# Optimization experiments

Hardware: AMD Instinct MI355X
Metric: run time of the kernel (lower is better)

The kernel has to match this reference:

```python
import jax, jax.numpy as jnp
import numpy as np

T, B, V, L = 2000, 64, 163, 200  # frames, batch, vocab (162 phonemes + blank), max label len
NEG = -1e30  # log-space 'zero'
BLANK = 0


def _logaddexp3(a, b, c):
    m = jnp.maximum(jnp.maximum(a, b), c)
    return m + jnp.log(jnp.exp(a - m) + jnp.exp(b - m) + jnp.exp(c - m))


def _ctc_single(logp, labels, act_len, label_len):
    # logp: [T, V] log-probs for one utterance; labels: [L] ints in [1, V)
    Tt, _ = logp.shape
    Ll = labels.shape[0]
    S = 2 * Ll + 1  # extended label: blank, l1, blank, l2, ..., blank
    s = jnp.arange(S)
    ext = jnp.where(s % 2 == 1, labels[jnp.minimum((s - 1) // 2, Ll - 1)], BLANK)
    valid = s < 2 * label_len + 1
    ext_m2 = jnp.concatenate([jnp.full((2,), -1, ext.dtype), ext[:-2]])
    allow_skip = (ext != BLANK) & (ext != ext_m2)

    alpha0 = jnp.where((s < 2) & valid, logp[0, ext], NEG)

    def step(alpha, tlp):
        t, lp = tlp
        sh1 = jnp.concatenate([jnp.full((1,), NEG, alpha.dtype), alpha[:-1]])
        sh2 = jnp.concatenate([jnp.full((2,), NEG, alpha.dtype), alpha[:-2]])
        sh2 = jnp.where(allow_skip, sh2, NEG)
        new = _logaddexp3(alpha, sh1, sh2) + lp[ext]
        new = jnp.where(valid, new, NEG)
        new = jnp.where(t < act_len, new, alpha)  # freeze past this utterance's length
        return new, None

    ts = jnp.arange(1, Tt)
    alpha, _ = jax.lax.scan(step, alpha0, (ts, logp[1:]))

    end = 2 * label_len  # index of final blank
    a_last = alpha[end]
    a_prev = jnp.where(label_len > 0, alpha[jnp.maximum(end - 1, 0)], NEG)
    m = jnp.maximum(a_last, a_prev)
    ll = m + jnp.log(jnp.exp(a_last - m) + jnp.exp(a_prev - m))
    return -ll  # negative log-likelihood


def setup_inputs() -> dict:
    key = jax.random.key(0)
    k1, k2, k3, k4 = jax.random.split(key, 4)
    logits = jax.random.normal(k1, (T, B, V), dtype=jnp.float32)
    # labels in [1, V): module does IntTensor(concat(phonemes)) + 1, blank = 0
    labels = jax.random.randint(k2, (B, L), 0, V - 1, dtype=jnp.int32) + 1
    label_lens = jax.random.randint(k3, (B,), L // 2, L + 1, dtype=jnp.int32)
    act_lens = jax.random.randint(k4, (B,), T // 2, T + 1, dtype=jnp.int32)
    # module enforces act_len > label_len (always true here: >=1000 vs <=200)
    return {"logits": logits, "labels": labels, "act_lens": act_lens, "label_lens": label_lens}


def reference(logits, labels, act_lens, label_lens):
    # warp-ctc applies softmax internally over the vocab axis
    logp = jax.nn.log_softmax(logits, axis=-1)          # [T, B, V]
    logp_b = jnp.transpose(logp, (1, 0, 2))             # [B, T, V]
    losses = jax.vmap(_ctc_single)(logp_b, labels, act_lens, label_lens)  # [B]
    # warp-ctc length_average=True: sum of losses / total number of frames
    total = jnp.sum(losses) / jnp.sum(act_lens).astype(losses.dtype)
    return total
```

## Files before the change

kernel.cpp:

```cpp
#include <hip/hip_runtime.h>
#include <math.h>

#define T_FRAMES 2000
#define B_BATCH  64
#define V_VOCAB  163
#define L_MAX    200
#define SPT      8
#define EBIAS    320
#define PFD      8
#define GROW     260

#define L2E 1.4426950408889634f
#define LN2D 0.6931471805599453

typedef float f4 __attribute__((ext_vector_type(4)));

__device__ __forceinline__ float wave_reduce_max(float v) {
#pragma unroll
  for (int i = 1; i < 64; i <<= 1) v = fmaxf(v, __shfl_xor(v, i, 64));
  return v;
}
__device__ __forceinline__ float wave_reduce_sum(float v) {
#pragma unroll
  for (int i = 1; i < 64; i <<= 1) v += __shfl_xor(v, i, 64);
  return v;
}
__device__ __forceinline__ int wave_reduce_max_i(int v) {
#pragma unroll
  for (int i = 1; i < 64; i <<= 1) v = max(v, __shfl_xor(v, i, 64));
  return v;
}
__device__ __forceinline__ double wave_reduce_sum_d(double v) {
#pragma unroll
  for (int i = 1; i < 64; i <<= 1) v += __shfl_xor(v, i, 64);
  return v;
}

__global__ __launch_bounds__(256) void softmax_expand_kernel(const float* __restrict__ logits,
                                                             const int* __restrict__ labels,
                                                             float* __restrict__ G) {
  int r = blockIdx.x * 4 + (threadIdx.x >> 6);
  int lane = threadIdx.x & 63;
  int w = threadIdx.x >> 6;
  int b = r / T_FRAMES;
  int t = r - b * T_FRAMES;
  const float* __restrict__ src = logits + ((size_t)t * B_BATCH + b) * V_VOCAB;
  float x0 = (lane < V_VOCAB) ? src[lane] : -1e30f;
  float x1 = (lane + 64 < V_VOCAB) ? src[lane + 64] : -1e30f;
  float x2 = (lane + 128 < V_VOCAB) ? src[lane + 128] : -1e30f;
  float e0 = exp2f(fmaf(x0, L2E, -12.0f));
  float e1 = exp2f(fmaf(x1, L2E, -12.0f));
  float e2 = exp2f(fmaf(x2, L2E, -12.0f));
  float inv = 1.0f / wave_reduce_sum(e0 + e1 + e2);

  __shared__ float pl[4][V_VOCAB];
  if (lane < V_VOCAB) pl[w][lane] = e0 * inv;
  if (lane + 64 < V_VOCAB) pl[w][lane + 64] = e1 * inv;
  if (lane + 128 < V_VOCAB) pl[w][lane + 128] = e2 * inv;
  __syncthreads();

  const int* __restrict__ lb = labels + b * L_MAX;
  float* __restrict__ dst = G + (size_t)r * GROW;
  int k0 = lane * 4;
  f4 o;
#pragma unroll
  for (int i = 0; i < 4; ++i) {
    int k = k0 + i;
    int kc = (k < L_MAX) ? k : (L_MAX - 1);
    o[i] = pl[w][lb[kc]];
  }
  *(f4*)(dst + k0) = o;
  if (lane == 0) dst[256] = pl[w][0];
}

__global__ __launch_bounds__(256) void lse_kernel(const float* __restrict__ logits,
                                                  float* __restrict__ lse2) {
  int row = blockIdx.x * 4 + (threadIdx.x >> 6);
  if (row >= T_FRAMES * B_BATCH) return;
  int lane = threadIdx.x & 63;
  const float* __restrict__ src = logits + (size_t)row * V_VOCAB;
  float x0 = (lane < V_VOCAB) ? src[lane] : -1e30f;
  float x1 = (lane + 64 < V_VOCAB) ? src[lane + 64] : -1e30f;
  float x2 = (lane + 128 < V_VOCAB) ? src[lane + 128] : -1e30f;
  float mx = wave_reduce_max(fmaxf(fmaxf(x0, x1), x2));
  float ssum = wave_reduce_sum(exp2f((x0 - mx) * L2E) + exp2f((x1 - mx) * L2E) +
                               exp2f((x2 - mx) * L2E));
  if (lane == 0) lse2[row] = mx * L2E + log2f(ssum);
}

__device__ __forceinline__ void gload4(f4& dst, int voff, const float* sbase) {
  asm volatile("global_load_dwordx4 %0, %1, %2"
               : "=v"(dst)
               : "v"(voff), "s"(sbase));
}
__device__ __forceinline__ void gload1(float& dst, int voff, const float* sbase) {
  asm volatile("global_load_dword %0, %1, %2"
               : "=v"(dst)
               : "v"(voff), "s"(sbase));
}
template <int N>
__device__ __forceinline__ void wait_row2(f4& q, float& bl) {
  asm volatile("s_waitcnt vmcnt(%2)" : "+v"(q), "+v"(bl) : "i"(N));
}
template <int N>
__device__ __forceinline__ void wait_row3(f4& q, float& bl, float& p4) {
  asm volatile("s_waitcnt vmcnt(%3)" : "+v"(q), "+v"(bl), "+v"(p4) : "i"(N));
}

__global__ __launch_bounds__(64, 1) void ctc_bidir_kernel(const float* __restrict__ G,
                                                          const int* __restrict__ labels,
                                                          const int* __restrict__ act_lens,
                                                          const int* __restrict__ label_lens,
                                                          double* __restrict__ Am,
                                                          double* __restrict__ Bm,
                                                          int* __restrict__ LSa,
                                                          int* __restrict__ LSb) {
  const int bid = blockIdx.x;
  const bool fwd = bid < B_BATCH;
  const int b = fwd ? bid : bid - B_BATCH;
  const int lane = threadIdx.x;
  const int act_len = act_lens[b];
  const int LL = label_lens[b];
  const int send = 2 * LL;
  const int tm = act_len >> 1;
  const int* __restrict__ lb = labels + b * L_MAX;
  const float* __restrict__ base = G + (size_t)b * T_FRAMES * GROW;

  const int voff4 = lane * 16;
  const int voffb = 256 * 4;
  const int voffp = lane * 16 + 16;

  f4 Q[PFD];
  float BL[PFD];
  double a[SPT];
  int LS = 0;

  if (fwd) {
    double m2o[4];
#pragma unroll
    for (int jj = 0; jj < 4; ++jj) {
      int k = 4 * lane + jj;
      int kc = (k < L_MAX) ? k : (L_MAX - 1);
      int kp = (k - 1 < L_MAX) ? (k - 1) : (L_MAX - 1);
      m2o[jj] = (k >= 1 && lb[kc] != lb[kp]) ? 1.0 : 0.0;
    }
    const double m10 = (lane == 0) ? 0.0 : 1.0;

#pragma unroll
    for (int j = 0; j < SPT; ++j) a[j] = 0.0;
    if (lane == 0) {
      a[0] = (double)base[256];
      a[1] = (double)base[0];
    }
    asm volatile("s_waitcnt vmcnt(0)" ::: "memory");

    const float* bp = base + GROW;
    const float* bhi = base + (size_t)(T_FRAMES - 1) * GROW;
    auto issue = [&](int p) {
      const float* rp = (bp > bhi) ? bhi : bp;
      gload4(Q[p], voff4, rp);
      gload1(BL[p], voffb, rp);
      bp += GROW;
    };

    double prev1;
    auto step = [&](int p) {
      double B = (double)BL[p];
      double p1 = (double)Q[p][0], p3 = (double)Q[p][1];
      double p5 = (double)Q[p][2], p7 = (double)Q[p][3];
      double n6 = (a[6] + a[5]) * B;
      double n7 = fma(m2o[3], a[5], a[7] + a[6]) * p7;
      double np1 = __shfl_up(n7, 1, 64);
      double n0 = fma(m10, prev1, a[0]) * B;
      double n1 = fma(m2o[0], prev1, a[1] + a[0]) * p1;
      double n2 = (a[2] + a[1]) * B;
      double n3 = fma(m2o[1], a[1], a[3] + a[2]) * p3;
      double n4 = (a[4] + a[3]) * B;
      double n5 = fma(m2o[2], a[3], a[5] + a[4]) * p5;
      a[0] = n0; a[1] = n1; a[2] = n2; a[3] = n3;
      a[4] = n4; a[5] = n5; a[6] = n6; a[7] = n7;
      prev1 = np1;
    };
    auto renorm = [&]() {
      double m = a[0];
#pragma unroll
      for (int j = 1; j < SPT; ++j) m = fmax(m, a[j]);
      int eb = (int)(__double_as_longlong(m) >> 52);
      eb = wave_reduce_max_i(eb);
      int sc = (eb - 1022) - EBIAS;
#pragma unroll
      for (int j = 0; j < SPT; ++j) a[j] = ldexp(a[j], -sc);
      prev1 = ldexp(prev1, -sc);
      LS += sc;
    };

#pragma unroll
    for (int d = 0; d < PFD; ++d) issue(d);
    prev1 = __shfl_up(a[7], 1, 64);

    const int nf = tm;
    int t = 0;
    while (t + 4 * PFD <= nf) {
#pragma unroll
      for (int u = 0; u < 4; ++u)
#pragma unroll
        for (int p = 0; p < PFD; ++p) { wait_row2<14>(Q[p], BL[p]); step(p); issue(p); }
      t += 4 * PFD;
      renorm();
    }
    while (t + PFD <= nf) {
#pragma unroll
      for (int p = 0; p < PFD; ++p) { wait_row2<14>(Q[p], BL[p]); step(p); issue(p); }
      t += PFD;
      renorm();
    }
    {
      int R = nf - t;
      if (R > 0) { wait_row2<14>(Q[0], BL[0]); step(0); }
      if (R > 1) { wait_row2<12>(Q[1], BL[1]); step(1); }
      if (R > 2) { wait_row2<10>(Q[2], BL[2]); step(2); }
      if (R > 3) { wait_row2<8>(Q[3], BL[3]); step(3); }
      if (R > 4) { wait_row2<6>(Q[4], BL[4]); step(4); }
      if (R > 5) { wait_row2<4>(Q[5], BL[5]); step(5); }
      if (R > 6) { wait_row2<2>(Q[6], BL[6]); step(6); }
    }
    asm volatile("s_waitcnt vmcnt(0)" ::: "memory");

#pragma unroll
    for (int j = 0; j < SPT; ++j) Am[(size_t)b * 512 + lane * SPT + j] = a[j];
    if (lane == 0) LSa[b] = LS;
  } else {
    float P4[PFD];
    double mdo[4];
#pragma unroll
    for (int jj = 0; jj < 4; ++jj) {
      int k = 4 * lane + jj + 1;
      int kc = (k < L_MAX) ? k : (L_MAX - 1);
      int kp = (k - 1 < L_MAX) ? (k - 1) : (L_MAX - 1);
      mdo[jj] = (lb[kc] != lb[kp]) ? 1.0 : 0.0;
    }

#pragma unroll
    for (int j = 0; j < SPT; ++j) a[j] = 0.0;
    if (lane == (send >> 3)) a[send & 7] = 1.0;
    if (lane == ((send - 1) >> 3)) a[(send - 1) & 7] = 1.0;
    asm volatile("s_waitcnt vmcnt(0)" ::: "memory");

    const float* bp = base + (size_t)(act_len - 1) * GROW;
    auto issue = [&](int p) {
      const float* rp = (bp < base) ? base : bp;
      gload4(Q[p], voff4, rp);
      gload1(BL[p], voffb, rp);
      gload1(P4[p], voffp, rp);
      bp -= GROW;
    };

    const bool l63 = (lane == 63);
    double a0n, a1n;
    {
      double t0 = __shfl_down(a[0], 1, 64);
      double t1 = __shfl_down(a[1], 1, 64);
      a0n = l63 ? 0.0 : t0;
      a1n = l63 ? 0.0 : t1;
    }

    auto step = [&](int p) {
      double B = (double)BL[p];
      double p1 = (double)Q[p][0], p3 = (double)Q[p][1];
      double p5 = (double)Q[p][2], p7 = (double)Q[p][3];
      double p9 = (double)P4[p];
      double g0 = a[0] * B;
      double g1 = a[1] * p1;
      double g2 = a[2] * B;
      double g3 = a[3] * p3;
      double na0 = g0 + g1;
      double na1 = fma(mdo[0], g3, g1 + g2);
      double t0 = __shfl_down(na0, 1, 64);
      double t1 = __shfl_down(na1, 1, 64);
      double gn0 = a0n * B;
      double gn1 = a1n * p9;
      double g4 = a[4] * B;
      double g5 = a[5] * p5;
      double g6 = a[6] * B;
      double g7 = a[7] * p7;
      a[0] = na0;
      a[1] = na1;
      a[2] = g2 + g3;
      a[3] = fma(mdo[1], g5, g3 + g4);
      a[4] = g4 + g5;
      a[5] = fma(mdo[2], g7, g5 + g6);
      a[6] = g6 + g7;
      a[7] = fma(mdo[3], gn1, g7 + gn0);
      a0n = l63 ? 0.0 : t0;
      a1n = l63 ? 0.0 : t1;
    };
    auto renorm = [&]() {
      double m = a[0];
#pragma unroll
      for (int j = 1; j < SPT; ++j) m = fmax(m, a[j]);
      int eb = (int)(__double_as_longlong(m) >> 52);
      eb = wave_reduce_max_i(eb);
      int sc = (eb - 1022) - EBIAS;
#pragma unroll
      for (int j = 0; j < SPT; ++j) a[j] = ldexp(a[j], -sc);
      a0n = ldexp(a0n, -sc);
      a1n = ldexp(a1n, -sc);
      LS += sc;
    };

#pragma unroll
    for (int d = 0; d < PFD; ++d) issue(d);

    const int nb = act_len - 1 - tm;
    int t = 0;
    while (t + 4 * PFD <= nb) {
#pragma unroll
      for (int u = 0; u < 4; ++u)
#pragma unroll
        for (int p = 0; p < PFD; ++p) { wait_row3<21>(Q[p], BL[p], P4[p]); step(p); issue(p); }
      t += 4 * PFD;
      renorm();
    }
    while (t + PFD <= nb) {
#pragma unroll
      for (int p = 0; p < PFD; ++p) { wait_row3<21>(Q[p], BL[p], P4[p]); step(p); issue(p); }
      t += PFD;
      renorm();
    }
    {
      int R = nb - t;
      if (R > 0) { wait_row3<21>(Q[0], BL[0], P4[0]); step(0); }
      if (R > 1) { wait_row3<18>(Q[1], BL[1], P4[1]); step(1); }
      if (R > 2) { wait_row3<15>(Q[2], BL[2], P4[2]); step(2); }
      if (R > 3) { wait_row3<12>(Q[3], BL[3], P4[3]); step(3); }
      if (R > 4) { wait_row3<9>(Q[4], BL[4], P4[4]); step(4); }
      if (R > 5) { wait_row3<6>(Q[5], BL[5], P4[5]); step(5); }
      if (R > 6) { wait_row3<3>(Q[6], BL[6], P4[6]); step(6); }
    }
    asm volatile("s_waitcnt vmcnt(0)" ::: "memory");

#pragma unroll
    for (int j = 0; j < SPT; ++j) Bm[(size_t)b * 512 + lane * SPT + j] = a[j];
    if (lane == 0) LSb[b] = LS;
  }
}

__global__ __launch_bounds__(64) void combine_kernel(const double* __restrict__ Am,
                                                     const double* __restrict__ Bm,
                                                     const int* __restrict__ LSa,
                                                     const int* __restrict__ LSb,
                                                     float* __restrict__ losses) {
  int b = blockIdx.x;
  int lane = threadIdx.x;
  double s = 0.0;
#pragma unroll
  for (int j = 0; j < SPT; ++j) {
    size_t idx = (size_t)b * 512 + lane * SPT + j;
    s += Am[idx] * Bm[idx];
  }
  s = wave_reduce_sum_d(s);
  if (lane == 0)
    losses[b] = (float)(-(log2(s) + (double)(LSa[b] + LSb[b])) * LN2D);
}

#define SPT7 7
__global__ __launch_bounds__(64, 1) void ctc_kernel_lse(const float* __restrict__ mat,
                                                        const float* __restrict__ lse2,
                                                        const int* __restrict__ labels,
                                                        const int* __restrict__ act_lens,
                                                        const int* __restrict__ label_lens,
                                                        float* __restrict__ losses) {
  const int b = blockIdx.x;
  const int lane = threadIdx.x;
  const int act_len = act_lens[b];
  const int LL = label_lens[b];
  const int send = 2 * LL;
  const int* __restrict__ lb = labels + b * L_MAX;

  int off[SPT7];
  double m2[SPT7];
#pragma unroll
  for (int j = 0; j < SPT7; ++j) {
    int s = lane * SPT7 + j;
    bool odd = (s & 1) != 0;
    int k = odd ? ((s - 1) >> 1) : 0;
    int kc = (k < L_MAX) ? k : (L_MAX - 1);
    int lab = odd ? lb[kc] : 0;
    off[j] = lab;
    bool skip = odd && (k >= 1) && (lab != lb[kc - 1]);
    m2[j] = skip ? 1.0 : 0.0;
  }
  auto rowptr = [&](int row) -> const float* {
    return mat + ((size_t)row * B_BATCH + b) * V_VOCAB;
  };
  double a[SPT7];
  {
    const float* r0 = rowptr(0);
    float nls0 = -lse2[b];
#pragma unroll
    for (int j = 0; j < SPT7; ++j) {
      int s = lane * SPT7 + j;
      double p = 0.0;
      if (s < 2 && s <= send) p = (double)exp2f(fmaf(r0[off[j]], L2E, nls0));
      a[j] = p;
    }
  }
  double prev1, prev2;
  const bool l0 = (lane == 0);
  int LS = 0;
  {
    double np1 = __shfl_up(a[SPT7 - 1], 1, 64);
    double np2 = __shfl_up(a[SPT7 - 2], 1, 64);
    prev1 = l0 ? 0.0 : np1;
    prev2 = l0 ? 0.0 : np2;
  }
  for (int t = 1; t < act_len; ++t) {
    const float* rp = rowptr(t);
    float nls = -lse2[t * B_BATCH + b];
    double pv[SPT7];
#pragma unroll
    for (int j = 0; j < SPT7; ++j) pv[j] = (double)exp2f(fmaf(rp[off[j]], L2E, nls));
    double n5 = fma(m2[5], a[3], a[5] + a[4]) * pv[5];
    double n6 = fma(m2[6], a[4], a[6] + a[5]) * pv[6];
    double n0 = fma(m2[0], prev2, a[0] + prev1) * pv[0];
    double n1 = fma(m2[1], prev1, a[1] + a[0]) * pv[1];
    double n2 = fma(m2[2], a[0], a[2] + a[1]) * pv[2];
    double n3 = fma(m2[3], a[1], a[3] + a[2]) * pv[3];
    double n4 = fma(m2[4], a[2], a[4] + a[3]) * pv[4];
    a[5] = n5; a[6] = n6;
    double np1 = __shfl_up(a[6], 1, 64);
    double np2 = __shfl_up(a[5], 1, 64);
    a[0] = n0; a[1] = n1; a[2] = n2; a[3] = n3; a[4] = n4;
    prev1 = l0 ? 0.0 : np1;
    prev2 = l0 ? 0.0 : np2;
    if ((t & 7) == 0) {
      double m = a[0];
#pragma unroll
      for (int j = 1; j < SPT7; ++j) m = fmax(m, a[j]);
      int eb = (int)(__double_as_longlong(m) >> 52);
      eb = wave_reduce_max_i(eb);
      int sc = (eb - 1022) - EBIAS;
#pragma unroll
      for (int j = 0; j < SPT7; ++j) a[j] = ldexp(a[j], -sc);
      prev1 = ldexp(prev1, -sc);
      prev2 = ldexp(prev2, -sc);
      LS += sc;
    }
  }
  __shared__ double sh[64 * SPT7];
#pragma unroll
  for (int j = 0; j < SPT7; ++j) sh[lane * SPT7 + j] = a[j];
  __syncthreads();
  if (lane == 0) {
    double ae = sh[send];
    double ap = (LL > 0) ? sh[send - 1] : 0.0;
    losses[b] = (float)(-(log2(ae + ap) + (double)LS) * LN2D);
  }
}

__global__ __launch_bounds__(64) void finalize_kernel(const float* __restrict__ losses,
                                                      const int* __restrict__ act_lens,
                                                      float* __restrict__ out) {
  int lane = threadIdx.x;
  float l = losses[lane];
  float n = (float)act_lens[lane];
  l = wave_reduce_sum(l);
  n = wave_reduce_sum(n);
  if (lane == 0) out[0] = l / n;
}

extern "C" void kernel_launch(void* const* d_in, const int* in_sizes, int n_in,
                              void* d_out, int out_size, void* d_ws, size_t ws_size,
                              hipStream_t stream) {
  const float* logits = (const float*)d_in[0];
  const int* labels = (const int*)d_in[1];
  const int* act_lens = (const int*)d_in[2];
  const int* label_lens = (const int*)d_in[3];
  float* out = (float*)d_out;

  const size_t g_bytes = (size_t)B_BATCH * T_FRAMES * GROW * sizeof(float);
  const size_t mid_bytes = (size_t)B_BATCH * 512 * sizeof(double);
  const int rows = T_FRAMES * B_BATCH;
  const int sm_grid = rows / 4;

  if (ws_size >= g_bytes + 2 * mid_bytes + 4096) {
    char* w = (char*)d_ws;
    float* G = (float*)w;                 w += g_bytes;
    double* Am = (double*)w;              w += mid_bytes;
    double* Bm = (double*)w;              w += mid_bytes;
    int* LSa = (int*)w;                   w += 256;
    int* LSb = (int*)w;                   w += 256;
    float* losses = (float*)w;
    softmax_expand_kernel<<<dim3(sm_grid), dim3(256), 0, stream>>>(logits, labels, G);
    ctc_bidir_kernel<<<dim3(2 * B_BATCH), dim3(64), 0, stream>>>(G, labels, act_lens,
                                                                 label_lens, Am, Bm, LSa, LSb);
    combine_kernel<<<dim3(B_BATCH), dim3(64), 0, stream>>>(Am, Bm, LSa, LSb, losses);
    finalize_kernel<<<dim3(1), dim3(64), 0, stream>>>(losses, act_lens, out);
  } else {
    float* lse2 = (float*)d_ws;
    float* losses = (float*)((char*)d_ws + (size_t)rows * sizeof(float));
    lse_kernel<<<dim3(sm_grid), dim3(256), 0, stream>>>(logits, lse2);
    ctc_kernel_lse<<<dim3(B_BATCH), dim3(64), 0, stream>>>(logits, lse2, labels,
                                                           act_lens, label_lens, losses);
    finalize_kernel<<<dim3(1), dim3(64), 0, stream>>>(losses, act_lens, out);
  }
}
```

Measured before the change: 259.3 us.

## Store gathered label probabilities as fp16 to halve intermediate traffic

```diff
diff --git a/kernel.cpp b/kernel.cpp
--- a/kernel.cpp
+++ b/kernel.cpp
@@ -1,4 +1,5 @@
 #include <hip/hip_runtime.h>
+#include <hip/hip_fp16.h>
 #include <math.h>
 
 #define T_FRAMES 2000
@@ -6,14 +7,23 @@
 #define V_VOCAB  163
 #define L_MAX    200
 #define SPT      8
-#define EBIAS    320
+#define EBIAS    0
 #define PFD      8
-#define GROW     260
+#define GROWH    224
+#define PBIAS    16384.0f
 
 #define L2E 1.4426950408889634f
 #define LN2D 0.6931471805599453
 
-typedef float f4 __attribute__((ext_vector_type(4)));
+typedef unsigned int u2v __attribute__((ext_vector_type(2)));
+
+__device__ __forceinline__ float h2f(unsigned short us) {
+  __half_raw hr; hr.x = us;
+  return __half2float(__half(hr));
+}
+__device__ __forceinline__ unsigned short f2h(float f) {
+  return __half_as_ushort(__float2half_rn(f));
+}
 
 __device__ __forceinline__ float wave_reduce_max(float v) {
 #pragma unroll
@@ -38,7 +48,7 @@
 
 __global__ __launch_bounds__(256) void softmax_expand_kernel(const float* __restrict__ logits,
                                                              const int* __restrict__ labels,
-                                                             float* __restrict__ G) {
+                                                             unsigned short* __restrict__ G) {
   int r = blockIdx.x * 4 + (threadIdx.x >> 6);
   int lane = threadIdx.x & 63;
   int w = threadIdx.x >> 6;
@@ -51,7 +61,7 @@
   float e0 = exp2f(fmaf(x0, L2E, -12.0f));
   float e1 = exp2f(fmaf(x1, L2E, -12.0f));
   float e2 = exp2f(fmaf(x2, L2E, -12.0f));
-  float inv = 1.0f / wave_reduce_sum(e0 + e1 + e2);
+  float inv = PBIAS / wave_reduce_sum(e0 + e1 + e2);
 
   __shared__ float pl[4][V_VOCAB];
   if (lane < V_VOCAB) pl[w][lane] = e0 * inv;
@@ -60,17 +70,22 @@
   __syncthreads();
 
   const int* __restrict__ lb = labels + b * L_MAX;
-  float* __restrict__ dst = G + (size_t)r * GROW;
-  int k0 = lane * 4;
-  f4 o;
-#pragma unroll
-  for (int i = 0; i < 4; ++i) {
-    int k = k0 + i;
-    int kc = (k < L_MAX) ? k : (L_MAX - 1);
-    o[i] = pl[w][lb[kc]];
-  }
-  *(f4*)(dst + k0) = o;
-  if (lane == 0) dst[256] = pl[w][0];
+  unsigned short* __restrict__ dst = G + (size_t)r * GROWH;
+  if (lane < 50) {
+    int k0 = lane * 4;
+    unsigned short h0 = f2h(pl[w][lb[k0 + 0]]);
+    unsigned short h1 = f2h(pl[w][lb[k0 + 1]]);
+    unsigned short h2 = f2h(pl[w][lb[k0 + 2]]);
+    unsigned short h3 = f2h(pl[w][lb[k0 + 3]]);
+    u2v o;
+    o.x = (unsigned)h0 | ((unsigned)h1 << 16);
+    o.y = (unsigned)h2 | ((unsigned)h3 << 16);
+    *(u2v*)(dst + k0) = o;
+  } else if (lane < 56) {
+    u2v v; v.x = 0u; v.y = 0u;
+    if (lane == 50) v.x = (unsigned)f2h(pl[w][0]);
+    *(u2v*)(dst + 200 + (lane - 50) * 4) = v;
+  }
 }
 
 __global__ __launch_bounds__(256) void lse_kernel(const float* __restrict__ logits,
@@ -88,26 +103,26 @@
   if (lane == 0) lse2[row] = mx * L2E + log2f(ssum);
 }
 
-__device__ __forceinline__ void gload4(f4& dst, int voff, const float* sbase) {
-  asm volatile("global_load_dwordx4 %0, %1, %2"
+__device__ __forceinline__ void gload2(u2v& dst, int voff, const unsigned short* sbase) {
+  asm volatile("global_load_dwordx2 %0, %1, %2"
                : "=v"(dst)
                : "v"(voff), "s"(sbase));
 }
-__device__ __forceinline__ void gload1(float& dst, int voff, const float* sbase) {
+__device__ __forceinline__ void gload1u(unsigned int& dst, int voff, const unsigned short* sbase) {
   asm volatile("global_load_dword %0, %1, %2"
                : "=v"(dst)
                : "v"(voff), "s"(sbase));
 }
 template <int N>
-__device__ __forceinline__ void wait_row2(f4& q, float& bl) {
-  asm volatile("s_waitcnt vmcnt(%2)" : "+v"(q), "+v"(bl) : "i"(N));
+__device__ __forceinline__ void wait_q(u2v& q) {
+  asm volatile("s_waitcnt vmcnt(%1)" : "+v"(q) : "i"(N));
 }
 template <int N>
-__device__ __forceinline__ void wait_row3(f4& q, float& bl, float& p4) {
-  asm volatile("s_waitcnt vmcnt(%3)" : "+v"(q), "+v"(bl), "+v"(p4) : "i"(N));
-}
-
-__global__ __launch_bounds__(64, 1) void ctc_bidir_kernel(const float* __restrict__ G,
+__device__ __forceinline__ void wait_qp(u2v& q, unsigned int& p4) {
+  asm volatile("s_waitcnt vmcnt(%2)" : "+v"(q), "+v"(p4) : "i"(N));
+}
+
+__global__ __launch_bounds__(64, 1) void ctc_bidir_kernel(const unsigned short* __restrict__ G,
                                                           const int* __restrict__ labels,
                                                           const int* __restrict__ act_lens,
                                                           const int* __restrict__ label_lens,
@@ -124,14 +139,12 @@
   const int send = 2 * LL;
   const int tm = act_len >> 1;
   const int* __restrict__ lb = labels + b * L_MAX;
-  const float* __restrict__ base = G + (size_t)b * T_FRAMES * GROW;
-
-  const int voff4 = lane * 16;
-  const int voffb = 256 * 4;
-  const int voffp = lane * 16 + 16;
-
-  f4 Q[PFD];
-  float BL[PFD];
+  const unsigned short* __restrict__ base = G + (size_t)b * T_FRAMES * GROWH;
+
+  const int voffq = lane * 8;
+  const int voffp = lane * 8 + 8;
+
+  u2v Q[PFD];
   double a[SPT];
   int LS = 0;
 
@@ -149,25 +162,28 @@
 #pragma unroll
     for (int j = 0; j < SPT; ++j) a[j] = 0.0;
     if (lane == 0) {
-      a[0] = (double)base[256];
-      a[1] = (double)base[0];
+      a[0] = (double)h2f(base[200]);
+      a[1] = (double)h2f(base[0]);
     }
     asm volatile("s_waitcnt vmcnt(0)" ::: "memory");
 
-    const float* bp = base + GROW;
-    const float* bhi = base + (size_t)(T_FRAMES - 1) * GROW;
+    const unsigned short* bp = base + GROWH;
+    const unsigned short* bhi = base + (size_t)(T_FRAMES - 1) * GROWH;
     auto issue = [&](int p) {
-      const float* rp = (bp > bhi) ? bhi : bp;
-      gload4(Q[p], voff4, rp);
-      gload1(BL[p], voffb, rp);
-      bp += GROW;
+      const unsigned short* rp = (bp > bhi) ? bhi : bp;
+      gload2(Q[p], voffq, rp);
+      bp += GROWH;
     };
 
     double prev1;
     auto step = [&](int p) {
-      double B = (double)BL[p];
-      double p1 = (double)Q[p][0], p3 = (double)Q[p][1];
-      double p5 = (double)Q[p][2], p7 = (double)Q[p][3];
+      unsigned int lo = Q[p].x, hi = Q[p].y;
+      unsigned int blu = __builtin_amdgcn_readlane(lo, 50);
+      double B  = (double)h2f((unsigned short)blu);
+      double p1 = (double)h2f((unsigned short)lo);
+      double p3 = (double)h2f((unsigned short)(lo >> 16));
+      double p5 = (double)h2f((unsigned short)hi);
+      double p7 = (double)h2f((unsigned short)(hi >> 16));
       double n6 = (a[6] + a[5]) * B;
       double n7 = fma(m2o[3], a[5], a[7] + a[6]) * p7;
       double np1 = __shfl_up(n7, 1, 64);
@@ -185,7 +201,7 @@
       double m = a[0];
 #pragma unroll
       for (int j = 1; j < SPT; ++j) m = fmax(m, a[j]);
-      int eb = (int)(__double_as_longlong(m) >> 52);
+      int eb = (int)((__double_as_longlong(m) >> 52) & 0x7ff);
       eb = wave_reduce_max_i(eb);
       int sc = (eb - 1022) - EBIAS;
 #pragma unroll
@@ -204,33 +220,33 @@
 #pragma unroll
       for (int u = 0; u < 4; ++u)
 #pragma unroll
-        for (int p = 0; p < PFD; ++p) { wait_row2<14>(Q[p], BL[p]); step(p); issue(p); }
+        for (int p = 0; p < PFD; ++p) { wait_q<7>(Q[p]); step(p); issue(p); }
       t += 4 * PFD;
       renorm();
     }
     while (t + PFD <= nf) {
 #pragma unroll
-      for (int p = 0; p < PFD; ++p) { wait_row2<14>(Q[p], BL[p]); step(p); issue(p); }
+      for (int p = 0; p < PFD; ++p) { wait_q<7>(Q[p]); step(p); issue(p); }
       t += PFD;
       renorm();
     }
     {
       int R = nf - t;
-      if (R > 0) { wait_row2<14>(Q[0], BL[0]); step(0); }
-      if (R > 1) { wait_row2<12>(Q[1], BL[1]); step(1); }
-      if (R > 2) { wait_row2<10>(Q[2], BL[2]); step(2); }
-      if (R > 3) { wait_row2<8>(Q[3], BL[3]); step(3); }
-      if (R > 4) { wait_row2<6>(Q[4], BL[4]); step(4); }
-      if (R > 5) { wait_row2<4>(Q[5], BL[5]); step(5); }
-      if (R > 6) { wait_row2<2>(Q[6], BL[6]); step(6); }
+      if (R > 0) { wait_q<7>(Q[0]); step(0); }
+      if (R > 1) { wait_q<6>(Q[1]); step(1); }
+      if (R > 2) { wait_q<5>(Q[2]); step(2); }
+      if (R > 3) { wait_q<4>(Q[3]); step(3); }
+      if (R > 4) { wait_q<3>(Q[4]); step(4); }
+      if (R > 5) { wait_q<2>(Q[5]); step(5); }
+      if (R > 6) { wait_q<1>(Q[6]); step(6); }
     }
     asm volatile("s_waitcnt vmcnt(0)" ::: "memory");
 
 #pragma unroll
     for (int j = 0; j < SPT; ++j) Am[(size_t)b * 512 + lane * SPT + j] = a[j];
-    if (lane == 0) LSa[b] = LS;
+    if (lane == 0) LSa[b] = LS - 14 * (tm + 1);
   } else {
-    float P4[PFD];
+    unsigned int P4[PFD];
     double mdo[4];
 #pragma unroll
     for (int jj = 0; jj < 4; ++jj) {
@@ -246,13 +262,12 @@
     if (lane == ((send - 1) >> 3)) a[(send - 1) & 7] = 1.0;
     asm volatile("s_waitcnt vmcnt(0)" ::: "memory");
 
-    const float* bp = base + (size_t)(act_len - 1) * GROW;
+    const unsigned short* bp = base + (size_t)(act_len - 1) * GROWH;
     auto issue = [&](int p) {
-      const float* rp = (bp < base) ? base : bp;
-      gload4(Q[p], voff4, rp);
-      gload1(BL[p], voffb, rp);
-      gload1(P4[p], voffp, rp);
-      bp -= GROW;
+      const unsigned short* rp = (bp < base) ? base : bp;
+      gload2(Q[p], voffq, rp);
+      gload1u(P4[p], voffp, rp);
+      bp -= GROWH;
     };
 
     const bool l63 = (lane == 63);
@@ -265,10 +280,14 @@
     }
 
     auto step = [&](int p) {
-      double B = (double)BL[p];
-      double p1 = (double)Q[p][0], p3 = (double)Q[p][1];
-      double p5 = (double)Q[p][2], p7 = (double)Q[p][3];
-      double p9 = (double)P4[p];
+      unsigned int lo = Q[p].x, hi = Q[p].y;
+      unsigned int blu = __builtin_amdgcn_readlane(lo, 50);
+      double B  = (double)h2f((unsigned short)blu);
+      double p1 = (double)h2f((unsigned short)lo);
+      double p3 = (double)h2f((unsigned short)(lo >> 16));
+      double p5 = (double)h2f((unsigned short)hi);
+      double p7 = (double)h2f((unsigned short)(hi >> 16));
+      double p9 = (double)h2f((unsigned short)P4[p]);
       double g0 = a[0] * B;
       double g1 = a[1] * p1;
       double g2 = a[2] * B;
@@ -298,7 +317,7 @@
       double m = a[0];
 #pragma unroll
       for (int j = 1; j < SPT; ++j) m = fmax(m, a[j]);
-      int eb = (int)(__double_as_longlong(m) >> 52);
+      int eb = (int)((__double_as_longlong(m) >> 52) & 0x7ff);
       eb = wave_reduce_max_i(eb);
       int sc = (eb - 1022) - EBIAS;
 #pragma unroll
@@ -317,31 +336,31 @@
 #pragma unroll
       for (int u = 0; u < 4; ++u)
 #pragma unroll
-        for (int p = 0; p < PFD; ++p) { wait_row3<21>(Q[p], BL[p], P4[p]); step(p); issue(p); }
+        for (int p = 0; p < PFD; ++p) { wait_qp<14>(Q[p], P4[p]); step(p); issue(p); }
       t += 4 * PFD;
       renorm();
     }
     while (t + PFD <= nb) {
 #pragma unroll
-      for (int p = 0; p < PFD; ++p) { wait_row3<21>(Q[p], BL[p], P4[p]); step(p); issue(p); }
+      for (int p = 0; p < PFD; ++p) { wait_qp<14>(Q[p], P4[p]); step(p); issue(p); }
       t += PFD;
       renorm();
     }
     {
       int R = nb - t;
-      if (R > 0) { wait_row3<21>(Q[0], BL[0], P4[0]); step(0); }
-      if (R > 1) { wait_row3<18>(Q[1], BL[1], P4[1]); step(1); }
-      if (R > 2) { wait_row3<15>(Q[2], BL[2], P4[2]); step(2); }
-      if (R > 3) { wait_row3<12>(Q[3], BL[3], P4[3]); step(3); }
-      if (R > 4) { wait_row3<9>(Q[4], BL[4], P4[4]); step(4); }
-      if (R > 5) { wait_row3<6>(Q[5], BL[5], P4[5]); step(5); }
-      if (R > 6) { wait_row3<3>(Q[6], BL[6], P4[6]); step(6); }
+      if (R > 0) { wait_qp<14>(Q[0], P4[0]); step(0); }
+      if (R > 1) { wait_qp<12>(Q[1], P4[1]); step(1); }
+      if (R > 2) { wait_qp<10>(Q[2], P4[2]); step(2); }
+      if (R > 3) { wait_qp<8>(Q[3], P4[3]); step(3); }
+      if (R > 4) { wait_qp<6>(Q[4], P4[4]); step(4); }
+      if (R > 5) { wait_qp<4>(Q[5], P4[5]); step(5); }
+      if (R > 6) { wait_qp<2>(Q[6], P4[6]); step(6); }
     }
     asm volatile("s_waitcnt vmcnt(0)" ::: "memory");
 
 #pragma unroll
     for (int j = 0; j < SPT; ++j) Bm[(size_t)b * 512 + lane * SPT + j] = a[j];
-    if (lane == 0) LSb[b] = LS;
+    if (lane == 0) LSb[b] = LS - 14 * nb;
   }
 }
 
@@ -437,9 +456,9 @@
       double m = a[0];
 #pragma unroll
       for (int j = 1; j < SPT7; ++j) m = fmax(m, a[j]);
-      int eb = (int)(__double_as_longlong(m) >> 52);
+      int eb = (int)((__double_as_longlong(m) >> 52) & 0x7ff);
       eb = wave_reduce_max_i(eb);
-      int sc = (eb - 1022) - EBIAS;
+      int sc = (eb - 1022);
 #pragma unroll
       for (int j = 0; j < SPT7; ++j) a[j] = ldexp(a[j], -sc);
       prev1 = ldexp(prev1, -sc);
@@ -478,18 +497,18 @@
   const int* label_lens = (const int*)d_in[3];
   float* out = (float*)d_out;
 
-  const size_t g_bytes = (size_t)B_BATCH * T_FRAMES * GROW * sizeof(float);
+  const size_t g_bytes = (size_t)B_BATCH * T_FRAMES * GROWH * sizeof(unsigned short) + 1024;
   const size_t mid_bytes = (size_t)B_BATCH * 512 * sizeof(double);
   const int rows = T_FRAMES * B_BATCH;
   const int sm_grid = rows / 4;
 
   if (ws_size >= g_bytes + 2 * mid_bytes + 4096) {
     char* w = (char*)d_ws;
-    float* G = (float*)w;                 w += g_bytes;
-    double* Am = (double*)w;              w += mid_bytes;
-    double* Bm = (double*)w;              w += mid_bytes;
-    int* LSa = (int*)w;                   w += 256;
-    int* LSb = (int*)w;                   w += 256;
+    unsigned short* G = (unsigned short*)w;  w += g_bytes;
+    double* Am = (double*)w;                 w += mid_bytes;
+    double* Bm = (double*)w;                 w += mid_bytes;
+    int* LSa = (int*)w;                      w += 256;
+    int* LSb = (int*)w;                      w += 256;
     float* losses = (float*)w;
     softmax_expand_kernel<<<dim3(sm_grid), dim3(256), 0, stream>>>(logits, labels, G);
     ctc_bidir_kernel<<<dim3(2 * B_BATCH), dim3(64), 0, stream>>>(G, labels, act_lens,
```

Measured after the change: 259.4 us. Within noise of the previous version (+0.0%).
